# Performance work log

Measured on AMD Instinct MI355X. Metric: run time of the kernel, lower is better.

Reference implementation:

```python
import jax, jax.numpy as jnp
import numpy as np
import math

B, N, DIM, DEPTH, HEADS, DHEAD = 4, 8192, 256, 4, 8, 32
NB = int(DHEAD * math.log(DHEAD))  # 110 random features (performer_pytorch default)
INNER = HEADS * DHEAD  # 256


def _ortho_proj(rng, nb, d):
    # gaussian orthogonal random matrix, scaling=0 (row norms of a fresh gaussian)
    blocks = []
    for _ in range(-(-nb // d)):
        q, _ = np.linalg.qr(rng.standard_normal((d, d)))
        blocks.append(q.T)
    m = np.concatenate(blocks, 0)[:nb]
    mult = np.linalg.norm(rng.standard_normal((nb, d)), axis=1)
    return (mult[:, None] * m).astype(np.float32)


def setup_inputs() -> dict:
    rng = np.random.default_rng(0)
    p = lambda *s: jnp.asarray((rng.standard_normal(s) * 0.02).astype(np.float32))
    return {
        "x": jnp.asarray(rng.standard_normal((B, N, DIM)).astype(np.float32)),
        "proj": jnp.asarray(np.stack([_ortho_proj(rng, NB, DHEAD) for _ in range(DEPTH)])),
        "ln1_g": jnp.ones((DEPTH, DIM), jnp.float32),
        "ln1_b": jnp.zeros((DEPTH, DIM), jnp.float32),
        "Wq": p(DEPTH, DIM, INNER), "bq": jnp.zeros((DEPTH, INNER), jnp.float32),
        "Wk": p(DEPTH, DIM, INNER), "bk": jnp.zeros((DEPTH, INNER), jnp.float32),
        "Wv": p(DEPTH, DIM, INNER), "bv": jnp.zeros((DEPTH, INNER), jnp.float32),
        "Wo": p(DEPTH, INNER, DIM), "bo": jnp.zeros((DEPTH, DIM), jnp.float32),
        "ln2_g": jnp.ones((DEPTH, DIM), jnp.float32),
        "ln2_b": jnp.zeros((DEPTH, DIM), jnp.float32),
        "Wf1": p(DEPTH, DIM, 4 * DIM), "bf1": jnp.zeros((DEPTH, 4 * DIM), jnp.float32),
        "Wf2": p(DEPTH, 4 * DIM, DIM), "bf2": jnp.zeros((DEPTH, DIM), jnp.float32),
    }


def _ln(x, g, b):
    m = jnp.mean(x, axis=-1, keepdims=True)
    v = jnp.var(x, axis=-1, keepdims=True)
    return (x - m) * jax.lax.rsqrt(v + 1e-5) * g + b


def _softmax_kernel(x, proj, is_query, eps=1e-4):
    # FAVOR+ positive softmax-kernel feature map
    dn = x.shape[-1] ** -0.25
    ratio = proj.shape[0] ** -0.5
    xd = jnp.einsum('bhnd,md->bhnm', x * dn, proj)          # [b,h,n,nb]
    diag = jnp.sum(x * x, axis=-1, keepdims=True) * (0.5 * dn * dn)
    if is_query:
        mx = jnp.max(xd, axis=-1, keepdims=True)
    else:
        mx = jnp.max(xd, axis=(-2, -1), keepdims=True)
    mx = jax.lax.stop_gradient(mx)
    return ratio * (jnp.exp(xd - diag - mx) + eps)


def reference(x, proj, ln1_g, ln1_b, Wq, bq, Wk, bk, Wv, bv, Wo, bo,
              ln2_g, ln2_b, Wf1, bf1, Wf2, bf2):
    b, n, _ = x.shape
    h = x
    for i in range(DEPTH):
        # --- PreNorm FAVOR+ self-attention ---
        y = _ln(h, ln1_g[i], ln1_b[i])
        q = (y @ Wq[i] + bq[i]).reshape(b, n, HEADS, DHEAD).transpose(0, 2, 1, 3)
        k = (y @ Wk[i] + bk[i]).reshape(b, n, HEADS, DHEAD).transpose(0, 2, 1, 3)
        v = (y @ Wv[i] + bv[i]).reshape(b, n, HEADS, DHEAD).transpose(0, 2, 1, 3)
        qp = _softmax_kernel(q, proj[i], True)   # [b,h,n,nb]
        kp = _softmax_kernel(k, proj[i], False)  # [b,h,n,nb]
        d_inv = 1.0 / jnp.einsum('bhnm,bhm->bhn', qp, kp.sum(axis=2))
        ctx = jnp.einsum('bhnm,bhnd->bhmd', kp, v)          # [b,h,nb,d]
        o = jnp.einsum('bhnm,bhmd,bhn->bhnd', qp, ctx, d_inv)
        o = o.transpose(0, 2, 1, 3).reshape(b, n, INNER)
        h = h + o @ Wo[i] + bo[i]
        # --- PreNorm FFN ---
        y = _ln(h, ln2_g[i], ln2_b[i])
        h = h + jax.nn.gelu(y @ Wf1[i] + bf1[i]) @ Wf2[i] + bf2[i]
    return h
```

## Files before the change

kernel.cpp:

```cpp
#include <hip/hip_runtime.h>
#include <math.h>

#define NSEQ 8192
#define BATCH 4
#define DIM 256
#define HEADS 8
#define DHEAD 32
#define NB 110
#define INNER 256
#define FFDIM 1024
#define MROWS (BATCH * NSEQ)
#define BH (BATCH * HEADS)

typedef __attribute__((ext_vector_type(8))) short bf16x8;
typedef __attribute__((ext_vector_type(4))) short bf16x4;
typedef __attribute__((ext_vector_type(4))) float f32x4;

typedef __attribute__((address_space(1))) const void* gas_cvp;
typedef __attribute__((address_space(3))) void* las_vp;

constexpr float c_dn = 0.42044820762685725f;
constexpr float c_diagf = 0.08838834764831845f;
constexpr float c_ratio = 0.09534625892455922f;

__device__ __forceinline__ unsigned short f2b(float f) {
    unsigned u = __float_as_uint(f);
    unsigned r = (u + 0x7FFFu + ((u >> 16) & 1u)) >> 16;
    return (unsigned short)r;
}
__device__ __forceinline__ float b2f(unsigned short u) {
    return __uint_as_float((unsigned)u << 16);
}

__global__ __launch_bounds__(256) void copy4_kernel(const float4* __restrict__ src,
                                                    float4* __restrict__ dst, int n4) {
    int i = blockIdx.x * 256 + threadIdx.x;
    if (i < n4) dst[i] = src[i];
}
__global__ __launch_bounds__(256) void zero_kernel(float* __restrict__ p, int n) {
    int i = blockIdx.x * 256 + threadIdx.x;
    if (i < n) p[i] = 0.0f;
}
__global__ __launch_bounds__(256) void bcat_kernel(const float* __restrict__ bq,
                                                   const float* __restrict__ bk,
                                                   const float* __restrict__ bv,
                                                   float* __restrict__ out) {
    int l = blockIdx.x, t = threadIdx.x;
    out[l * 768 + t] = bq[l * 256 + t];
    out[l * 768 + 256 + t] = bk[l * 256 + t];
    out[l * 768 + 512 + t] = bv[l * 256 + t];
}

__global__ __launch_bounds__(256) void ln_kernel(const float* __restrict__ x,
                                                 const float* __restrict__ g,
                                                 const float* __restrict__ bta,
                                                 unsigned short* __restrict__ y) {
    int wave = threadIdx.x >> 6, lane = threadIdx.x & 63;
    int row = blockIdx.x * 4 + wave;
    const float* xr = x + (size_t)row * DIM;
    float4 v = *(const float4*)(xr + lane * 4);
    float s = v.x + v.y + v.z + v.w;
    float sq = v.x * v.x + v.y * v.y + v.z * v.z + v.w * v.w;
    #pragma unroll
    for (int off = 32; off; off >>= 1) {
        s += __shfl_xor(s, off);
        sq += __shfl_xor(sq, off);
    }
    float mean = s * (1.0f / DIM);
    float var = sq * (1.0f / DIM) - mean * mean;
    float rstd = rsqrtf(var + 1e-5f);
    float4 gg = *(const float4*)(g + lane * 4);
    float4 bb = *(const float4*)(bta + lane * 4);
    bf16x4 o;
    o[0] = (short)f2b((v.x - mean) * rstd * gg.x + bb.x);
    o[1] = (short)f2b((v.y - mean) * rstd * gg.y + bb.y);
    o[2] = (short)f2b((v.z - mean) * rstd * gg.z + bb.z);
    o[3] = (short)f2b((v.w - mean) * rstd * gg.w + bb.w);
    *(bf16x4*)(y + (size_t)row * DIM + lane * 4) = o;
}

__global__ __launch_bounds__(256) void wt_kernel(const float* __restrict__ in,
                                                 unsigned short* __restrict__ out,
                                                 int K, int Nn, int lstride) {
    __shared__ float t32[32][33];
    int l = blockIdx.z;
    const float* inp = in + (size_t)l * K * Nn;
    unsigned short* outp = out + (size_t)l * lstride;
    int k0 = blockIdx.x * 32, n0 = blockIdx.y * 32;
    int tx = threadIdx.x & 31, ty = threadIdx.x >> 5;
    #pragma unroll
    for (int i = 0; i < 4; ++i)
        t32[ty + i * 8][tx] = inp[(size_t)(k0 + ty + i * 8) * Nn + n0 + tx];
    __syncthreads();
    #pragma unroll
    for (int i = 0; i < 4; ++i) {
        int r = ty + i * 8;
        outp[(size_t)(n0 + r) * K + k0 + tx] = f2b(t32[tx][r]);
    }
}

template <int EPI>
__global__ __launch_bounds__(256) void gemm_mfma(const unsigned short* __restrict__ A,
                                                 const unsigned short* __restrict__ Wt,
                                                 const float* __restrict__ bias,
                                                 const float* __restrict__ res,
                                                 void* __restrict__ Cv,
                                                 int Nn, int K) {
    __shared__ __align__(16) unsigned short pool[24576];
    unsigned short* AsP = pool;
    unsigned short* BsP = pool + 12288;
    int tid = threadIdx.x;
    int nwg = gridDim.x * gridDim.y;
    int orig = blockIdx.y * gridDim.x + blockIdx.x;
    int swz = (orig & 7) * (nwg >> 3) + (orig >> 3);
    int m0 = (swz / gridDim.x) * 128, n0 = (swz % gridDim.x) * 128;
    int wave = tid >> 6, lane = tid & 63;
    int wm = (wave >> 1) * 64, wn = (wave & 1) * 64;
    int lr = lane & 15, lg = lane >> 4;
    f32x4 acc[4][4];
    #pragma unroll
    for (int i = 0; i < 4; ++i)
        #pragma unroll
        for (int j = 0; j < 4; ++j) acc[i][j] = (f32x4){0.f, 0.f, 0.f, 0.f};

    int rowS[2], chS[2];
    #pragma unroll
    for (int j = 0; j < 2; ++j) {
        int f = wave * 128 + j * 64 + lane;
        rowS[j] = f >> 2;
        chS[j] = ((f & 3) ^ ((rowS[j] >> 1) & 3)) * 8;
    }
    int rdA[4], rdB[4];
    #pragma unroll
    for (int i = 0; i < 4; ++i) {
        int ra = wm + i * 16 + lr;
        rdA[i] = ra * 32 + (lg ^ ((ra >> 1) & 3)) * 8;
        int rb = wn + i * 16 + lr;
        rdB[i] = rb * 32 + (lg ^ ((rb >> 1) & 3)) * 8;
    }

    const int NT = K >> 5;
    #pragma unroll
    for (int t = 0; t < 2; ++t) {
        #pragma unroll
        for (int j = 0; j < 2; ++j) {
            const unsigned short* srcA = A + (size_t)(m0 + rowS[j]) * K + t * 32 + chS[j];
            __builtin_amdgcn_global_load_lds((gas_cvp)srcA,
                                             (las_vp)(AsP + t * 4096 + wave * 1024 + j * 512), 16, 0, 0);
            const unsigned short* srcB = Wt + (size_t)(n0 + rowS[j]) * K + t * 32 + chS[j];
            __builtin_amdgcn_global_load_lds((gas_cvp)srcB,
                                             (las_vp)(BsP + t * 4096 + wave * 1024 + j * 512), 16, 0, 0);
        }
    }
    int buf = 0;
    for (int kt = 0; kt < NT; ++kt) {
        if (kt + 2 < NT) {
            int nb = (kt + 2) % 3;
            int koff = (kt + 2) * 32;
            #pragma unroll
            for (int j = 0; j < 2; ++j) {
                const unsigned short* srcA = A + (size_t)(m0 + rowS[j]) * K + koff + chS[j];
                __builtin_amdgcn_global_load_lds((gas_cvp)srcA,
                                                 (las_vp)(AsP + nb * 4096 + wave * 1024 + j * 512), 16, 0, 0);
                const unsigned short* srcB = Wt + (size_t)(n0 + rowS[j]) * K + koff + chS[j];
                __builtin_amdgcn_global_load_lds((gas_cvp)srcB,
                                                 (las_vp)(BsP + nb * 4096 + wave * 1024 + j * 512), 16, 0, 0);
            }
        }
        int ahead = NT - 1 - kt;
        if (ahead >= 2)      asm volatile("s_waitcnt vmcnt(8)" ::: "memory");
        else if (ahead == 1) asm volatile("s_waitcnt vmcnt(4)" ::: "memory");
        else                 asm volatile("s_waitcnt vmcnt(0)" ::: "memory");
        __builtin_amdgcn_s_barrier();
        __builtin_amdgcn_sched_barrier(0);
        bf16x8 af[4], bfv[4];
        #pragma unroll
        for (int i = 0; i < 4; ++i) af[i] = *(bf16x8*)&AsP[buf * 4096 + rdA[i]];
        #pragma unroll
        for (int j = 0; j < 4; ++j) bfv[j] = *(bf16x8*)&BsP[buf * 4096 + rdB[j]];
        #pragma unroll
        for (int i = 0; i < 4; ++i)
            #pragma unroll
            for (int j = 0; j < 4; ++j)
                acc[i][j] = __builtin_amdgcn_mfma_f32_16x16x32_bf16(af[i], bfv[j], acc[i][j], 0, 0, 0);
        __builtin_amdgcn_sched_barrier(0);
        __builtin_amdgcn_s_barrier();
        buf = (buf + 1 == 3) ? 0 : buf + 1;
    }

    if (EPI == 1) {
        #pragma unroll
        for (int i = 0; i < 4; ++i) {
            #pragma unroll
            for (int j = 0; j < 4; ++j) {
                int col = n0 + wn + j * 16 + lr;
                float bv = bias[col];
                #pragma unroll
                for (int r = 0; r < 4; ++r) {
                    int row = m0 + wm + i * 16 + lg * 4 + r;
                    float c = acc[i][j][r] + bv + res[(size_t)row * Nn + col];
                    ((float*)Cv)[(size_t)row * Nn + col] = c;
                }
            }
        }
    } else {
        #pragma unroll
        for (int i = 0; i < 4; ++i) {
            #pragma unroll
            for (int j = 0; j < 4; ++j) {
                int tcol = wn + j * 16 + lr;
                float bv = bias[n0 + tcol];
                #pragma unroll
                for (int r = 0; r < 4; ++r) {
                    int trow = wm + i * 16 + lg * 4 + r;
                    float c = acc[i][j][r] + bv;
                    if (EPI == 2) {
                        float u = c;
                        float t = 1.5957691216057308f * (u + 0.044715f * u * u * u);
                        c = u / (1.0f + __expf(-t));
                    }
                    pool[trow * 128 + (((tcol >> 3) ^ (trow & 7)) << 3) + (tcol & 7)] = f2b(c);
                }
            }
        }
        __syncthreads();
        #pragma unroll
        for (int cch = 0; cch < 8; ++cch) {
            int g = cch * 256 + tid;
            int row = g >> 4, cc = g & 15;
            bf16x8 val = *(bf16x8*)&pool[row * 128 + ((cc ^ (row & 7)) << 3)];
            int grow = m0 + row;
            int gcol = n0 + cc * 8;
            if (EPI == 3) {
                size_t idx = (size_t)(gcol >> 8) * ((size_t)MROWS * DIM) + (size_t)grow * 256 + (gcol & 255);
                *(bf16x8*)((unsigned short*)Cv + idx) = val;
            } else {
                *(bf16x8*)((unsigned short*)Cv + (size_t)grow * Nn + gcol) = val;
            }
        }
    }
}

__global__ __launch_bounds__(256) void kmaxg_kernel(const unsigned short* __restrict__ k,
                                                    const float* __restrict__ proj,
                                                    float* __restrict__ partial) {
    __shared__ unsigned short As[128][40];
    __shared__ unsigned short Pj[112][40];
    __shared__ float wmax[4][8];
    int tid = threadIdx.x;
    int r0 = blockIdx.x * 128;
    for (int idx = tid; idx < 112 * 8; idx += 256) {
        int m = idx >> 3, f4 = idx & 7;
        if (m < NB) {
            float4 va = *(const float4*)(proj + m * 32 + f4 * 4);
            bf16x4 pk = {(short)f2b(va.x), (short)f2b(va.y), (short)f2b(va.z), (short)f2b(va.w)};
            *(bf16x4*)&Pj[m][f4 * 4] = pk;
        } else {
            *(bf16x4*)&Pj[m][f4 * 4] = (bf16x4){0, 0, 0, 0};
        }
    }
    int arow = tid >> 1, ahalf = tid & 1;
    const unsigned short* ap = k + (size_t)(r0 + arow) * 32 + ahalf * 16;
    *(bf16x8*)&As[arow][ahalf * 16] = *(const bf16x8*)ap;
    *(bf16x8*)&As[arow][ahalf * 16 + 8] = *(const bf16x8*)(ap + 8);
    __syncthreads();
    int wave = tid >> 6, lane = tid & 63, lr = lane & 15, lg = lane >> 4;
    float mymax[4] = {-1e30f, -1e30f, -1e30f, -1e30f};
    #pragma unroll
    for (int mt = 0; mt < 2; ++mt) {
        bf16x8 af = *(bf16x8*)&As[(2 * wave + mt) * 16 + lr][lg * 8];
        #pragma unroll
        for (int nt = 0; nt < 7; ++nt) {
            bf16x8 bfp = *(bf16x8*)&Pj[nt * 16 + lr][lg * 8];
            f32x4 d = (f32x4){0.f, 0.f, 0.f, 0.f};
            d = __builtin_amdgcn_mfma_f32_16x16x32_bf16(af, bfp, d, 0, 0, 0);
            if (!(nt == 6 && lr >= 14)) {
                #pragma unroll
                for (int r = 0; r < 4; ++r) mymax[r] = fmaxf(mymax[r], d[r]);
            }
        }
    }
    #pragma unroll
    for (int r = 0; r < 4; ++r) {
        float v = mymax[r];
        v = fmaxf(v, __shfl_xor(v, 1));
        v = fmaxf(v, __shfl_xor(v, 2));
        v = fmaxf(v, __shfl_xor(v, 4));
        v = fmaxf(v, __shfl_xor(v, 8));
        v = fmaxf(v, __shfl_xor(v, 32));
        mymax[r] = v;
    }
    if (lane == 0 || lane == 16) {
        int hb = (lane >> 4) & 1;
        #pragma unroll
        for (int r = 0; r < 4; ++r) wmax[wave][4 * hb + r] = mymax[r];
    }
    __syncthreads();
    if (tid < 8) {
        float m = fmaxf(fmaxf(wmax[0][tid], wmax[1][tid]), fmaxf(wmax[2][tid], wmax[3][tid]));
        partial[blockIdx.x * 8 + tid] = m * c_dn;
    }
}

__global__ __launch_bounds__(256) void kreduce_kernel(const float* __restrict__ partial,
                                                      float* __restrict__ kmaxf) {
    __shared__ float wred[4];
    int bh = blockIdx.x, b = bh >> 3, h = bh & 7;
    int tid = threadIdx.x;
    float m = fmaxf(partial[(b * 512 + tid) * 8 + h], partial[(b * 512 + 256 + tid) * 8 + h]);
    #pragma unroll
    for (int off = 32; off; off >>= 1) m = fmaxf(m, __shfl_xor(m, off));
    if ((tid & 63) == 0) wred[tid >> 6] = m;
    __syncthreads();
    if (tid == 0)
        kmaxf[bh] = fmaxf(fmaxf(wred[0], wred[1]), fmaxf(wred[2], wred[3]));
}

__global__ __launch_bounds__(256) void ctxg_kernel(const unsigned short* __restrict__ k,
                                                   const unsigned short* __restrict__ v,
                                                   const float* __restrict__ proj,
                                                   const float* __restrict__ kmaxf,
                                                   float* __restrict__ ctx) {
    __shared__ __align__(16) char pool[34816];
    unsigned short (*As)[40] = (unsigned short(*)[40])pool;
    unsigned short (*KpT)[136] = (unsigned short(*)[136])pool;
    __shared__ unsigned short Pj[112][40];
    __shared__ unsigned short VsT[48][136];
    __shared__ float dg[128];
    int tid = threadIdx.x;
    int bh = blockIdx.y, b = bh >> 3, h = bh & 7;
    int n_base = blockIdx.x * 512;
    float mx = kmaxf[bh];
    for (int idx = tid; idx < 112 * 8; idx += 256) {
        int m = idx >> 3, f4 = idx & 7;
        if (m < NB) {
            float4 va = *(const float4*)(proj + m * 32 + f4 * 4);
            bf16x4 pk = {(short)f2b(va.x), (short)f2b(va.y), (short)f2b(va.z), (short)f2b(va.w)};
            *(bf16x4*)&Pj[m][f4 * 4] = pk;
        } else {
            *(bf16x4*)&Pj[m][f4 * 4] = (bf16x4){0, 0, 0, 0};
        }
    }
    for (int idx = tid; idx < 16 * 136; idx += 256) KpT[112 + idx / 136][idx % 136] = 0;
    for (int idx = tid; idx < 16 * 128; idx += 256) {
        int rr = 32 + (idx >> 7), nn = idx & 127;
        VsT[rr][nn] = (rr == 32) ? (unsigned short)0x3F80 : (unsigned short)0;
    }
    int wave = tid >> 6, lane = tid & 63, lr = lane & 15, lg = lane >> 4;
    int arow = tid >> 1, ahalf = tid & 1;
    f32x4 ctxacc[2][3];
    #pragma unroll
    for (int mt = 0; mt < 2; ++mt)
        #pragma unroll
        for (int nt = 0; nt < 3; ++nt) ctxacc[mt][nt] = (f32x4){0.f, 0.f, 0.f, 0.f};

    for (int ni = 0; ni < 4; ++ni) {
        int n0 = n_base + ni * 128;
        {
            const unsigned short* kp_ = k + ((size_t)(b * NSEQ + n0 + arow) * 256 + h * 32 + ahalf * 16);
            bf16x8 k0 = *(const bf16x8*)kp_;
            bf16x8 k1 = *(const bf16x8*)(kp_ + 8);
            *(bf16x8*)&As[arow][ahalf * 16] = k0;
            *(bf16x8*)&As[arow][ahalf * 16 + 8] = k1;
            float ssq = 0.f;
            #pragma unroll
            for (int e = 0; e < 8; ++e) {
                float a = b2f((unsigned short)k0[e]), bb = b2f((unsigned short)k1[e]);
                ssq += a * a + bb * bb;
            }
            ssq += __shfl_xor(ssq, 1);
            if (ahalf == 0) dg[arow] = ssq * c_diagf;
        }
        #pragma unroll
        for (int it = 0; it < 4; ++it) {
            int idx = it * 256 + tid;
            int nn = idx >> 3, f4 = idx & 7;
            bf16x4 vv = *(const bf16x4*)(v + ((size_t)(b * NSEQ + n0 + nn) * 256 + h * 32 + f4 * 4));
            VsT[f4 * 4 + 0][nn] = (unsigned short)vv[0];
            VsT[f4 * 4 + 1][nn] = (unsigned short)vv[1];
            VsT[f4 * 4 + 2][nn] = (unsigned short)vv[2];
            VsT[f4 * 4 + 3][nn] = (unsigned short)vv[3];
        }
        __syncthreads();
        f32x4 xds[2][7];
        #pragma unroll
        for (int mt = 0; mt < 2; ++mt) {
            bf16x8 af = *(bf16x8*)&As[(2 * wave + mt) * 16 + lr][lg * 8];
            #pragma unroll
            for (int nt = 0; nt < 7; ++nt) {
                bf16x8 bfp = *(bf16x8*)&Pj[nt * 16 + lr][lg * 8];
                f32x4 d = (f32x4){0.f, 0.f, 0.f, 0.f};
                xds[mt][nt] = __builtin_amdgcn_mfma_f32_16x16x32_bf16(af, bfp, d, 0, 0, 0);
            }
        }
        __syncthreads();
        #pragma unroll
        for (int mt = 0; mt < 2; ++mt)
            #pragma unroll
            for (int nt = 0; nt < 7; ++nt) {
                int m = nt * 16 + lr;
                #pragma unroll
                for (int r = 0; r < 4; ++r) {
                    int nn = (2 * wave + mt) * 16 + lg * 4 + r;
                    float kpv = (m < NB) ? c_ratio * (__expf(xds[mt][nt][r] * c_dn - dg[nn] - mx) + 1e-4f) : 0.f;
                    KpT[m][nn] = f2b(kpv);
                }
            }
        __syncthreads();
        #pragma unroll
        for (int ks = 0; ks < 4; ++ks)
            #pragma unroll
            for (int mt = 0; mt < 2; ++mt) {
                bf16x8 af2 = *(bf16x8*)&KpT[(2 * wave + mt) * 16 + lr][ks * 32 + lg * 8];
                #pragma unroll
                for (int nt = 0; nt < 3; ++nt) {
                    bf16x8 bf2v = *(bf16x8*)&VsT[nt * 16 + lr][ks * 32 + lg * 8];
                    ctxacc[mt][nt] = __builtin_amdgcn_mfma_f32_16x16x32_bf16(af2, bf2v, ctxacc[mt][nt], 0, 0, 0);
                }
            }
        __syncthreads();
    }
    #pragma unroll
    for (int mt = 0; mt < 2; ++mt)
        #pragma unroll
        for (int nt = 0; nt < 3; ++nt)
            #pragma unroll
            for (int r = 0; r < 4; ++r) {
                int m = (2 * wave + mt) * 16 + lg * 4 + r;
                atomicAdd(&ctx[((size_t)bh * 128 + m) * 48 + nt * 16 + lr], ctxacc[mt][nt][r]);
            }
}

__global__ __launch_bounds__(256) void og_kernel(const unsigned short* __restrict__ q,
                                                 const float* __restrict__ proj,
                                                 const float* __restrict__ ctx,
                                                 unsigned short* __restrict__ o) {
    __shared__ __align__(16) char pool[34816];
    unsigned short (*As)[40] = (unsigned short(*)[40])pool;
    unsigned short (*Qp)[136] = (unsigned short(*)[136])pool;
    __shared__ unsigned short Pj[112][40];
    __shared__ unsigned short CsT[48][136];
    __shared__ float dg[128];
    int tid = threadIdx.x;
    int bh = blockIdx.x >> 6, b = bh >> 3, h = bh & 7;
    int n0 = (blockIdx.x & 63) * 128;
    for (int idx = tid; idx < 112 * 8; idx += 256) {
        int m = idx >> 3, f4 = idx & 7;
        if (m < NB) {
            float4 va = *(const float4*)(proj + m * 32 + f4 * 4);
            bf16x4 pk = {(short)f2b(va.x), (short)f2b(va.y), (short)f2b(va.z), (short)f2b(va.w)};
            *(bf16x4*)&Pj[m][f4 * 4] = pk;
        } else {
            *(bf16x4*)&Pj[m][f4 * 4] = (bf16x4){0, 0, 0, 0};
        }
    }
    for (int idx = tid; idx < 128 * 12; idx += 256) {
        int m = idx / 12, c4 = idx - m * 12;
        float4 cv = *(const float4*)(ctx + ((size_t)bh * 128 + m) * 48 + c4 * 4);
        CsT[c4 * 4 + 0][m] = f2b(cv.x);
        CsT[c4 * 4 + 1][m] = f2b(cv.y);
        CsT[c4 * 4 + 2][m] = f2b(cv.z);
        CsT[c4 * 4 + 3][m] = f2b(cv.w);
    }
    int arow = tid >> 1, ahalf = tid & 1;
    {
        const unsigned short* qp_ = q + ((size_t)(b * NSEQ + n0 + arow) * 256 + h * 32 + ahalf * 16);
        bf16x8 q0 = *(const bf16x8*)qp_;
        bf16x8 q1 = *(const bf16x8*)(qp_ + 8);
        *(bf16x8*)&As[arow][ahalf * 16] = q0;
        *(bf16x8*)&As[arow][ahalf * 16 + 8] = q1;
        float ssq = 0.f;
        #pragma unroll
        for (int e = 0; e < 8; ++e) {
            float a = b2f((unsigned short)q0[e]), bb = b2f((unsigned short)q1[e]);
            ssq += a * a + bb * bb;
        }
        ssq += __shfl_xor(ssq, 1);
        if (ahalf == 0) dg[arow] = ssq * c_diagf;
    }
    __syncthreads();
    int wave = tid >> 6, lane = tid & 63, lr = lane & 15, lg = lane >> 4;
    f32x4 xds[2][7];
    #pragma unroll
    for (int mt = 0; mt < 2; ++mt) {
        bf16x8 af = *(bf16x8*)&As[(2 * wave + mt) * 16 + lr][lg * 8];
        #pragma unroll
        for (int nt = 0; nt < 7; ++nt) {
            bf16x8 bfp = *(bf16x8*)&Pj[nt * 16 + lr][lg * 8];
            f32x4 d = (f32x4){0.f, 0.f, 0.f, 0.f};
            xds[mt][nt] = __builtin_amdgcn_mfma_f32_16x16x32_bf16(af, bfp, d, 0, 0, 0);
        }
    }
    float rmax[2][4];
    #pragma unroll
    for (int mt = 0; mt < 2; ++mt)
        #pragma unroll
        for (int r = 0; r < 4; ++r) {
            float mv = -1e30f;
            #pragma unroll
            for (int nt = 0; nt < 7; ++nt)
                if (!(nt == 6 && lr >= 14)) mv = fmaxf(mv, xds[mt][nt][r]);
            mv = fmaxf(mv, __shfl_xor(mv, 1));
            mv = fmaxf(mv, __shfl_xor(mv, 2));
            mv = fmaxf(mv, __shfl_xor(mv, 4));
            mv = fmaxf(mv, __shfl_xor(mv, 8));
            rmax[mt][r] = mv;
        }
    __syncthreads();
    #pragma unroll
    for (int mt = 0; mt < 2; ++mt)
        #pragma unroll
        for (int r = 0; r < 4; ++r) {
            int row = (2 * wave + mt) * 16 + lg * 4 + r;
            #pragma unroll
            for (int nt = 0; nt < 7; ++nt) {
                int m = nt * 16 + lr;
                float qpv = (m < NB)
                    ? c_ratio * (__expf((xds[mt][nt][r] - rmax[mt][r]) * c_dn - dg[row]) + 1e-4f)
                    : 0.f;
                Qp[row][m] = f2b(qpv);
            }
            Qp[row][112 + lr] = 0;
        }
    __syncthreads();
    f32x4 oacc[2][3];
    #pragma unroll
    for (int mt = 0; mt < 2; ++mt)
        #pragma unroll
        for (int nt = 0; nt < 3; ++nt) oacc[mt][nt] = (f32x4){0.f, 0.f, 0.f, 0.f};
    #pragma unroll
    for (int ks = 0; ks < 4; ++ks)
        #pragma unroll
        for (int mt = 0; mt < 2; ++mt) {
            bf16x8 af2 = *(bf16x8*)&Qp[(2 * wave + mt) * 16 + lr][ks * 32 + lg * 8];
            #pragma unroll
            for (int nt = 0; nt < 3; ++nt) {
                bf16x8 bf2v = *(bf16x8*)&CsT[nt * 16 + lr][ks * 32 + lg * 8];
                oacc[mt][nt] = __builtin_amdgcn_mfma_f32_16x16x32_bf16(af2, bf2v, oacc[mt][nt], 0, 0, 0);
            }
        }
    #pragma unroll
    for (int mt = 0; mt < 2; ++mt)
        #pragma unroll
        for (int r = 0; r < 4; ++r) {
            int row = (2 * wave + mt) * 16 + lg * 4 + r;
            int n = n0 + row;
            float den = __shfl(oacc[mt][2][r], lane & 48);
            float inv = 1.0f / den;
            size_t base = (size_t)(b * NSEQ + n) * 256 + h * 32;
            o[base + lr] = f2b(oacc[mt][0][r] * inv);
            o[base + 16 + lr] = f2b(oacc[mt][1][r] * inv);
        }
}

extern "C" void kernel_launch(void* const* d_in, const int* in_sizes, int n_in,
                              void* d_out, int out_size, void* d_ws, size_t ws_size,
                              hipStream_t stream) {
    const float* x = (const float*)d_in[0];
    const float* proj = (const float*)d_in[1];
    const float* ln1_g = (const float*)d_in[2];
    const float* ln1_b = (const float*)d_in[3];
    const float* Wq = (const float*)d_in[4];
    const float* bq = (const float*)d_in[5];
    const float* Wk = (const float*)d_in[6];
    const float* bk = (const float*)d_in[7];
    const float* Wv = (const float*)d_in[8];
    const float* bv = (const float*)d_in[9];
    const float* Wo = (const float*)d_in[10];
    const float* bo = (const float*)d_in[11];
    const float* ln2_g = (const float*)d_in[12];
    const float* ln2_b = (const float*)d_in[13];
    const float* Wf1 = (const float*)d_in[14];
    const float* bf1 = (const float*)d_in[15];
    const float* Wf2 = (const float*)d_in[16];
    const float* bf2 = (const float*)d_in[17];

    float* h = (float*)d_out;
    const size_t ACT = (size_t)MROWS * DIM;
    unsigned short* y = (unsigned short*)d_ws;
    unsigned short* q = y + ACT;
    unsigned short* k = q + ACT;
    unsigned short* v = k + ACT;
    unsigned short* mid = v + ACT;
    float* ctx = (float*)(mid + 4 * ACT);
    float* kmaxf = ctx + (size_t)BH * 128 * 48;
    float* partial = kmaxf + 32;
    float* bqkv = partial + 2048 * 8;
    unsigned short* wt = (unsigned short*)(bqkv + 4 * 768);
    unsigned short* o = y;

    const int WT_L = 786432;
    const int CTXN = BH * 128 * 48;

    copy4_kernel<<<(int)(ACT / 4) / 256, 256, 0, stream>>>((const float4*)x, (float4*)h, (int)(ACT / 4));

    wt_kernel<<<dim3(8, 8, 4), 256, 0, stream>>>(Wq, wt + 0, 256, 256, WT_L);
    wt_kernel<<<dim3(8, 8, 4), 256, 0, stream>>>(Wk, wt + 65536, 256, 256, WT_L);
    wt_kernel<<<dim3(8, 8, 4), 256, 0, stream>>>(Wv, wt + 131072, 256, 256, WT_L);
    wt_kernel<<<dim3(8, 8, 4), 256, 0, stream>>>(Wo, wt + 196608, 256, 256, WT_L);
    wt_kernel<<<dim3(8, 32, 4), 256, 0, stream>>>(Wf1, wt + 262144, 256, 1024, WT_L);
    wt_kernel<<<dim3(32, 8, 4), 256, 0, stream>>>(Wf2, wt + 524288, 1024, 256, WT_L);
    bcat_kernel<<<4, 256, 0, stream>>>(bq, bk, bv, bqkv);

    for (int i = 0; i < 4; ++i) {
        const float* proj_i = proj + (size_t)i * NB * DHEAD;
        const unsigned short* wl = wt + (size_t)i * WT_L;
        ln_kernel<<<MROWS / 4, 256, 0, stream>>>(h, ln1_g + i * DIM, ln1_b + i * DIM, y);
        gemm_mfma<3><<<dim3(6, 256), 256, 0, stream>>>(y, wl + 0, bqkv + i * 768, nullptr, q, 768, DIM);

        zero_kernel<<<(CTXN + 255) / 256, 256, 0, stream>>>(ctx, CTXN);
        kmaxg_kernel<<<2048, 256, 0, stream>>>(k, proj_i, partial);
        kreduce_kernel<<<BH, 256, 0, stream>>>(partial, kmaxf);
        ctxg_kernel<<<dim3(16, BH), 256, 0, stream>>>(k, v, proj_i, kmaxf, ctx);
        og_kernel<<<BH * 64, 256, 0, stream>>>(q, proj_i, ctx, o);

        gemm_mfma<1><<<dim3(2, 256), 256, 0, stream>>>(o, wl + 196608, bo + i * DIM, h, h, DIM, INNER);

        ln_kernel<<<MROWS / 4, 256, 0, stream>>>(h, ln2_g + i * DIM, ln2_b + i * DIM, y);
        gemm_mfma<2><<<dim3(8, 256), 256, 0, stream>>>(y, wl + 262144, bf1 + i * FFDIM, nullptr, mid, FFDIM, DIM);
        gemm_mfma<1><<<dim3(2, 256), 256, 0, stream>>>(mid, wl + 524288, bf2 + i * DIM, h, h, DIM, FFDIM);
    }
}
```

Before: 848.6 us.

## Fuse residual-add GEMMs with following LayerNorm via full-row 64x256 tiles

Adds a gemm_ln kernel in which each workgroup computes a full 256-wide output row block (64 rows), so it can add bias and residual and then compute the LayerNorm statistics in registers with lane shuffles. It writes both the fp32 residual stream and the bf16 normalized activations, which removes the separate LN kernels after the Wo and Wf2 GEMMs. The first LN is hoisted before the layer loop. Only 512 workgroups each carry a 64x256 tile with double buffering, which may reduce occupancy and parallelism compared with the old 128x128 tiling.

```diff
diff --git a/kernel.cpp b/kernel.cpp
--- a/kernel.cpp
+++ b/kernel.cpp
@@ -188,54 +188,163 @@
         buf = (buf + 1 == 3) ? 0 : buf + 1;
     }
 
-    if (EPI == 1) {
-        #pragma unroll
-        for (int i = 0; i < 4; ++i) {
+    #pragma unroll
+    for (int i = 0; i < 4; ++i) {
+        #pragma unroll
+        for (int j = 0; j < 4; ++j) {
+            int tcol = wn + j * 16 + lr;
+            float bv = bias[n0 + tcol];
+            #pragma unroll
+            for (int r = 0; r < 4; ++r) {
+                int trow = wm + i * 16 + lg * 4 + r;
+                float c = acc[i][j][r] + bv;
+                if (EPI == 2) {
+                    float u = c;
+                    float t = 1.5957691216057308f * (u + 0.044715f * u * u * u);
+                    c = u / (1.0f + __expf(-t));
+                }
+                pool[trow * 128 + (((tcol >> 3) ^ (trow & 7)) << 3) + (tcol & 7)] = f2b(c);
+            }
+        }
+    }
+    __syncthreads();
+    #pragma unroll
+    for (int cch = 0; cch < 8; ++cch) {
+        int g = cch * 256 + tid;
+        int row = g >> 4, cc = g & 15;
+        bf16x8 val = *(bf16x8*)&pool[row * 128 + ((cc ^ (row & 7)) << 3)];
+        int grow = m0 + row;
+        int gcol = n0 + cc * 8;
+        if (EPI == 3) {
+            size_t idx = (size_t)(gcol >> 8) * ((size_t)MROWS * DIM) + (size_t)grow * 256 + (gcol & 255);
+            *(bf16x8*)((unsigned short*)Cv + idx) = val;
+        } else {
+            *(bf16x8*)((unsigned short*)Cv + (size_t)grow * Nn + gcol) = val;
+        }
+    }
+}
+
+template <int DO_LN>
+__global__ __launch_bounds__(256) void gemm_ln(const unsigned short* __restrict__ A,
+                                               const unsigned short* __restrict__ Wt,
+                                               const float* __restrict__ bias,
+                                               const float* __restrict__ res,
+                                               float* __restrict__ hout,
+                                               unsigned short* __restrict__ yout,
+                                               const float* __restrict__ gam,
+                                               const float* __restrict__ bet,
+                                               int K) {
+    __shared__ __align__(16) unsigned short As[2][64 * 32];
+    __shared__ __align__(16) unsigned short Bs[2][256 * 32];
+    int tid = threadIdx.x;
+    int nwg = gridDim.y;
+    int orig = blockIdx.y;
+    int swz = (orig & 7) * (nwg >> 3) + (orig >> 3);
+    int m0 = swz * 64;
+    int wave = tid >> 6, lane = tid & 63;
+    int lr = lane & 15, lg = lane >> 4;
+
+    f32x4 acc[16];
+    #pragma unroll
+    for (int j = 0; j < 16; ++j) acc[j] = (f32x4){0.f, 0.f, 0.f, 0.f};
+
+    int fA = wave * 64 + lane;
+    int rowA = fA >> 2, chA = ((fA & 3) ^ ((rowA >> 1) & 3)) * 8;
+    int rowB[4], chB[4];
+    #pragma unroll
+    for (int j = 0; j < 4; ++j) {
+        int f = wave * 256 + j * 64 + lane;
+        rowB[j] = f >> 2;
+        chB[j] = ((f & 3) ^ ((rowB[j] >> 1) & 3)) * 8;
+    }
+    int raA = wave * 16 + lr;
+    int rdAo = raA * 32 + (lg ^ ((raA >> 1) & 3)) * 8;
+    int rdBo[16];
+    #pragma unroll
+    for (int j = 0; j < 16; ++j) {
+        int rb = j * 16 + lr;
+        rdBo[j] = rb * 32 + (lg ^ ((rb >> 1) & 3)) * 8;
+    }
+
+    const int NT = K >> 5;
+    {
+        const unsigned short* srcA = A + (size_t)(m0 + rowA) * K + chA;
+        __builtin_amdgcn_global_load_lds((gas_cvp)srcA, (las_vp)(&As[0][wave * 512]), 16, 0, 0);
+        #pragma unroll
+        for (int j = 0; j < 4; ++j) {
+            const unsigned short* srcB = Wt + (size_t)rowB[j] * K + chB[j];
+            __builtin_amdgcn_global_load_lds((gas_cvp)srcB, (las_vp)(&Bs[0][wave * 2048 + j * 512]), 16, 0, 0);
+        }
+    }
+    for (int kt = 0; kt < NT; ++kt) {
+        int cur = kt & 1;
+        if (kt + 1 < NT) {
+            int nxt = cur ^ 1;
+            int koff = (kt + 1) * 32;
+            const unsigned short* srcA = A + (size_t)(m0 + rowA) * K + koff + chA;
+            __builtin_amdgcn_global_load_lds((gas_cvp)srcA, (las_vp)(&As[nxt][wave * 512]), 16, 0, 0);
             #pragma unroll
             for (int j = 0; j < 4; ++j) {
-                int col = n0 + wn + j * 16 + lr;
-                float bv = bias[col];
-                #pragma unroll
-                for (int r = 0; r < 4; ++r) {
-                    int row = m0 + wm + i * 16 + lg * 4 + r;
-                    float c = acc[i][j][r] + bv + res[(size_t)row * Nn + col];
-                    ((float*)Cv)[(size_t)row * Nn + col] = c;
-                }
-            }
-        }
-    } else {
-        #pragma unroll
-        for (int i = 0; i < 4; ++i) {
-            #pragma unroll
-            for (int j = 0; j < 4; ++j) {
-                int tcol = wn + j * 16 + lr;
-                float bv = bias[n0 + tcol];
-                #pragma unroll
-                for (int r = 0; r < 4; ++r) {
-                    int trow = wm + i * 16 + lg * 4 + r;
-                    float c = acc[i][j][r] + bv;
-                    if (EPI == 2) {
-                        float u = c;
-                        float t = 1.5957691216057308f * (u + 0.044715f * u * u * u);
-                        c = u / (1.0f + __expf(-t));
-                    }
-                    pool[trow * 128 + (((tcol >> 3) ^ (trow & 7)) << 3) + (tcol & 7)] = f2b(c);
-                }
-            }
-        }
-        __syncthreads();
-        #pragma unroll
-        for (int cch = 0; cch < 8; ++cch) {
-            int g = cch * 256 + tid;
-            int row = g >> 4, cc = g & 15;
-            bf16x8 val = *(bf16x8*)&pool[row * 128 + ((cc ^ (row & 7)) << 3)];
-            int grow = m0 + row;
-            int gcol = n0 + cc * 8;
-            if (EPI == 3) {
-                size_t idx = (size_t)(gcol >> 8) * ((size_t)MROWS * DIM) + (size_t)grow * 256 + (gcol & 255);
-                *(bf16x8*)((unsigned short*)Cv + idx) = val;
-            } else {
-                *(bf16x8*)((unsigned short*)Cv + (size_t)grow * Nn + gcol) = val;
+                const unsigned short* srcB = Wt + (size_t)rowB[j] * K + koff + chB[j];
+                __builtin_amdgcn_global_load_lds((gas_cvp)srcB, (las_vp)(&Bs[nxt][wave * 2048 + j * 512]), 16, 0, 0);
+            }
+            asm volatile("s_waitcnt vmcnt(5)" ::: "memory");
+        } else {
+            asm volatile("s_waitcnt vmcnt(0)" ::: "memory");
+        }
+        __builtin_amdgcn_s_barrier();
+        __builtin_amdgcn_sched_barrier(0);
+        bf16x8 af = *(bf16x8*)&As[cur][rdAo];
+        #pragma unroll
+        for (int j = 0; j < 16; ++j) {
+            bf16x8 bv = *(bf16x8*)&Bs[cur][rdBo[j]];
+            acc[j] = __builtin_amdgcn_mfma_f32_16x16x32_bf16(af, bv, acc[j], 0, 0, 0);
+        }
+        __builtin_amdgcn_sched_barrier(0);
+        __builtin_amdgcn_s_barrier();
+    }
+
+    float rs[4] = {0.f, 0.f, 0.f, 0.f};
+    float rq[4] = {0.f, 0.f, 0.f, 0.f};
+    #pragma unroll
+    for (int j = 0; j < 16; ++j) {
+        int col = j * 16 + lr;
+        float bv = bias[col];
+        #pragma unroll
+        for (int r = 0; r < 4; ++r) {
+            int row = m0 + wave * 16 + lg * 4 + r;
+            float c = acc[j][r] + bv + res[(size_t)row * 256 + col];
+            hout[(size_t)row * 256 + col] = c;
+            acc[j][r] = c;
+            if (DO_LN) { rs[r] += c; rq[r] += c * c; }
+        }
+    }
+    if (DO_LN) {
+        #pragma unroll
+        for (int r = 0; r < 4; ++r) {
+            float s = rs[r], sq = rq[r];
+            s += __shfl_xor(s, 1);  sq += __shfl_xor(sq, 1);
+            s += __shfl_xor(s, 2);  sq += __shfl_xor(sq, 2);
+            s += __shfl_xor(s, 4);  sq += __shfl_xor(sq, 4);
+            s += __shfl_xor(s, 8);  sq += __shfl_xor(sq, 8);
+            rs[r] = s; rq[r] = sq;
+        }
+        #pragma unroll
+        for (int r = 0; r < 4; ++r) {
+            float mean = rs[r] * (1.0f / 256.0f);
+            float var = rq[r] * (1.0f / 256.0f) - mean * mean;
+            rs[r] = mean;
+            rq[r] = rsqrtf(var + 1e-5f);
+        }
+        #pragma unroll
+        for (int j = 0; j < 16; ++j) {
+            int col = j * 16 + lr;
+            float gv = gam[col], bb = bet[col];
+            #pragma unroll
+            for (int r = 0; r < 4; ++r) {
+                int row = m0 + wave * 16 + lg * 4 + r;
+                float yv = (acc[j][r] - rs[r]) * rq[r] * gv + bb;
+                yout[(size_t)row * 256 + col] = f2b(yv);
             }
         }
     }
@@ -602,10 +711,11 @@
     wt_kernel<<<dim3(32, 8, 4), 256, 0, stream>>>(Wf2, wt + 524288, 1024, 256, WT_L);
     bcat_kernel<<<4, 256, 0, stream>>>(bq, bk, bv, bqkv);
 
+    ln_kernel<<<MROWS / 4, 256, 0, stream>>>(h, ln1_g, ln1_b, y);
+
     for (int i = 0; i < 4; ++i) {
         const float* proj_i = proj + (size_t)i * NB * DHEAD;
         const unsigned short* wl = wt + (size_t)i * WT_L;
-        ln_kernel<<<MROWS / 4, 256, 0, stream>>>(h, ln1_g + i * DIM, ln1_b + i * DIM, y);
         gemm_mfma<3><<<dim3(6, 256), 256, 0, stream>>>(y, wl + 0, bqkv + i * 768, nullptr, q, 768, DIM);
 
         zero_kernel<<<(CTXN + 255) / 256, 256, 0, stream>>>(ctx, CTXN);
@@ -614,10 +724,16 @@
         ctxg_kernel<<<dim3(16, BH), 256, 0, stream>>>(k, v, proj_i, kmaxf, ctx);
         og_kernel<<<BH * 64, 256, 0, stream>>>(q, proj_i, ctx, o);
 
-        gemm_mfma<1><<<dim3(2, 256), 256, 0, stream>>>(o, wl + 196608, bo + i * DIM, h, h, DIM, INNER);
-
-        ln_kernel<<<MROWS / 4, 256, 0, stream>>>(h, ln2_g + i * DIM, ln2_b + i * DIM, y);
+        gemm_ln<1><<<dim3(1, MROWS / 64), 256, 0, stream>>>(o, wl + 196608, bo + i * DIM, h, h, y,
+                                                            ln2_g + i * DIM, ln2_b + i * DIM, INNER);
+
         gemm_mfma<2><<<dim3(8, 256), 256, 0, stream>>>(y, wl + 262144, bf1 + i * FFDIM, nullptr, mid, FFDIM, DIM);
-        gemm_mfma<1><<<dim3(2, 256), 256, 0, stream>>>(mid, wl + 524288, bf2 + i * DIM, h, h, DIM, FFDIM);
-    }
-}
+        if (i < 3) {
+            gemm_ln<1><<<dim3(1, MROWS / 64), 256, 0, stream>>>(mid, wl + 524288, bf2 + i * DIM, h, h, y,
+                                                                ln1_g + (i + 1) * DIM, ln1_b + (i + 1) * DIM, FFDIM);
+        } else {
+            gemm_ln<0><<<dim3(1, MROWS / 64), 256, 0, stream>>>(mid, wl + 524288, bf2 + i * DIM, h, h, nullptr,
+                                                                nullptr, nullptr, FFDIM);
+        }
+    }
+}
```

New measurement: 850.2 us. Within noise of the previous version (+0.2%).
